# Kernel optimization log

Measured on AMD Instinct MI355X. Metric: run time of the kernel, lower is better.

## Reference

```python
import jax, jax.numpy as jnp
import numpy as np

HID = 128
FEAT = 16            # glob_in//(2+n_history) = (node_in-1)//4 = (edge_in-1)//4
N_GRAPHS = 512
N_NODES = 100000
N_EDGES = 400000
N_PER = 100000       # effects per branch (glob/node/edge)
A_TOTAL = 300000     # G.num_effects.sum()
EFF_PER_ACT = 4
NUM_ACTIONS = A_TOTAL // EFF_PER_ACT  # 75000 segments (static for jit)


def _lin(k, fan_in, fan_out):
    kw, kb = jax.random.split(k)
    s = 1.0 / np.sqrt(fan_in)
    W = jax.random.uniform(kw, (fan_in, fan_out), jnp.float32, -s, s)
    b = jax.random.uniform(kb, (fan_out,), jnp.float32, -s, s)
    return W, b


def setup_inputs() -> dict:
    key = jax.random.key(0)
    ks = jax.random.split(key, 16)
    globs = jax.random.normal(ks[0], (N_GRAPHS, HID), jnp.float32)
    nodes = jax.random.normal(ks[1], (N_NODES, HID), jnp.float32)
    edges = jax.random.normal(ks[2], (N_EDGES, HID), jnp.float32)
    action_globs = jax.random.normal(ks[3], (N_PER, FEAT), jnp.float32)
    action_nodes = jax.random.normal(ks[4], (N_PER, FEAT), jnp.float32)
    action_edges = jax.random.normal(ks[5], (N_PER, FEAT), jnp.float32)
    row = jax.random.randint(ks[6], (N_EDGES,), 0, N_NODES, jnp.int32)
    col = jax.random.randint(ks[7], (N_EDGES,), 0, N_NODES, jnp.int32)
    U = jax.random.randint(ks[8], (N_PER,), 0, N_GRAPHS, jnp.int32)
    V = jax.random.randint(ks[9], (N_PER,), 0, N_NODES, jnp.int32)
    E = jax.random.randint(ks[10], (N_PER,), 0, N_EDGES, jnp.int32)
    # disjoint write slots in the preallocated actions tensor
    UA = jnp.arange(N_PER, dtype=jnp.int32)
    VA = N_PER + jnp.arange(N_PER, dtype=jnp.int32)
    EA = 2 * N_PER + jnp.arange(N_PER, dtype=jnp.int32)
    # sorted per-effect action ids (4 effects per action)
    actions_batch = (jnp.arange(A_TOTAL, dtype=jnp.int32) // EFF_PER_ACT).astype(jnp.int32)
    glob_W, glob_b = _lin(ks[11], HID + FEAT, HID)
    node_W, node_b = _lin(ks[12], HID + FEAT, HID)
    e1_W, e1_b = _lin(ks[13], 2 * HID + FEAT, HID)
    e2_W, e2_b = _lin(ks[14], 2 * HID, HID)
    pol_W, pol_b = _lin(ks[15], HID, 1)
    return {
        "globs": globs, "nodes": nodes, "edges": edges,
        "action_globs": action_globs, "action_nodes": action_nodes, "action_edges": action_edges,
        "glob_W": glob_W, "glob_b": glob_b, "node_W": node_W, "node_b": node_b,
        "e1_W": e1_W, "e1_b": e1_b, "e2_W": e2_W, "e2_b": e2_b,
        "pol_W": pol_W, "pol_b": pol_b,
        "row": row, "col": col, "U": U, "UA": UA, "V": V, "VA": VA,
        "E": E, "EA": EA, "actions_batch": actions_batch,
    }


def _norm(batch):
    # torch norm(): consecutive group ids starting at batch[0]
    changed = (batch[1:] != batch[:-1]).astype(batch.dtype)
    return batch[0] + jnp.concatenate([jnp.zeros((1,), batch.dtype), jnp.cumsum(changed)])


def reference(globs, nodes, edges, action_globs, action_nodes, action_edges,
              glob_W, glob_b, node_W, node_b, e1_W, e1_b, e2_W, e2_b,
              pol_W, pol_b, row, col, U, UA, V, VA, E, EA, actions_batch):
    actions = jnp.zeros((A_TOTAL, HID), globs.dtype)
    # glob branch: gather globs -> small Linear -> index_put
    ga = jnp.concatenate([globs[U], action_globs], axis=1) @ glob_W + glob_b
    actions = actions.at[UA].set(ga)
    # node branch
    na = jnp.concatenate([nodes[V], action_nodes], axis=1) @ node_W + node_b
    actions = actions.at[VA].set(na)
    # edge branch: two chained Linears over gathered endpoint node feats
    EE = jnp.concatenate([nodes[row[E]], action_edges, nodes[col[E]]], axis=1) @ e1_W + e1_b
    ea = jnp.concatenate([edges[E], EE], axis=1) @ e2_W + e2_b
    actions = actions.at[EA].set(ea)
    # scatter_add segment reduction over action ids
    seg = _norm(actions_batch)
    agg = jax.ops.segment_sum(actions, seg, num_segments=NUM_ACTIONS)  # [NUM_ACTIONS, HID]
    return agg @ pol_W + pol_b  # [NUM_ACTIONS, 1]
```

## Files before the change

kernel.cpp:

```cpp
#include <hip/hip_runtime.h>

#define HID 128
#define FEAT 16
#define N_PER 100000
#define NUM_ACTIONS 75000
#define N_NODES 100000
#define N_GRAPHS 512

#define NSCAL_OFF 1024
#define GSCAL_OFF (NSCAL_OFF + 4 * N_NODES)
#define ESCAL_OFF (GSCAL_OFF + N_GRAPHS)
#define PSUM_OFF  (ESCAL_OFF + N_PER)

#define NB 760
#define EB 968
#define FB 288
#define GB 16
#define WORK_BLOCKS (NB + EB + FB + GB)

__device__ __forceinline__ float dot4(float4 a, float4 b) {
    return a.x * b.x + a.y * b.y + a.z * b.z + a.w * b.w;
}

template <int CTRL>
__device__ __forceinline__ float dpp_mov(float x) {
    return __int_as_float(__builtin_amdgcn_update_dpp(
        0, __float_as_int(x), CTRL, 0xF, 0xF, true));
}
__device__ __forceinline__ float red16(float x) {
    x += dpp_mov<0x111>(x);
    x += dpp_mov<0x112>(x);
    x += dpp_mov<0x114>(x);
    x += dpp_mov<0x118>(x);
    return x;
}
__device__ __forceinline__ float red32(float x) {
    x = red16(x);
    x += dpp_mov<0x142>(x);
    return x;
}
__device__ __forceinline__ float red64(float x) {
    x = red32(x);
    x += dpp_mov<0x143>(x);
    return x;
}

__global__ __launch_bounds__(1024) void fold_kernel(
    const float* __restrict__ glob_W, const float* __restrict__ glob_b,
    const float* __restrict__ node_W, const float* __restrict__ node_b,
    const float* __restrict__ e1_W,  const float* __restrict__ e1_b,
    const float* __restrict__ e2_W,  const float* __restrict__ e2_b,
    const float* __restrict__ pol_W, const float* __restrict__ pol_b,
    float* __restrict__ ws)
{
    __shared__ float qEE[HID];
    const int t = threadIdx.x, wave = t >> 6, lane = t & 63;
    const int bid = blockIdx.x;

    const bool needq = (bid >= 26 && bid <= 43);
    if (needq) {
        const int hw = t >> 5, s = t & 31;
        const float4 p4 = *(const float4*)&pol_W[4 * s];
        #pragma unroll
        for (int r = 0; r < 4; ++r) {
            const int k = hw + 32 * r;
            const float4 x = *(const float4*)&e2_W[(HID + k) * HID + 4 * s];
            float acc = red32(dot4(x, p4));
            if (s == 31) qEE[k] = acc;
        }
        __syncthreads();
    }

    const float2 p2 = *(const float2*)&pol_W[2 * lane];
    const int d = bid * 16 + wave;
    if (d == 691) {
        if (lane == 0) ws[691] = pol_b[0];
    } else if (d < 692) {
        float acc;
        if (d < 144) {
            const float2 x = *(const float2*)&glob_W[d * HID + 2 * lane];
            acc = x.x * p2.x + x.y * p2.y;
        } else if (d < 288) {
            const float2 x = *(const float2*)&node_W[(d - 144) * HID + 2 * lane];
            acc = x.x * p2.x + x.y * p2.y;
        } else if (d < 416) {
            const float2 x = *(const float2*)&e2_W[(d - 288) * HID + 2 * lane];
            acc = x.x * p2.x + x.y * p2.y;
        } else if (d < 688) {
            const float2 q2 = *(const float2*)&qEE[2 * lane];
            const float2 x  = *(const float2*)&e1_W[(d - 416) * HID + 2 * lane];
            acc = x.x * q2.x + x.y * q2.y;
        } else if (d == 688) {
            const float2 x = *(const float2*)&glob_b[2 * lane];
            acc = x.x * p2.x + x.y * p2.y;
        } else if (d == 689) {
            const float2 x = *(const float2*)&node_b[2 * lane];
            acc = x.x * p2.x + x.y * p2.y;
        } else {
            const float2 q2 = *(const float2*)&qEE[2 * lane];
            const float2 x1 = *(const float2*)&e1_b[2 * lane];
            const float2 x2 = *(const float2*)&e2_b[2 * lane];
            acc = x1.x * q2.x + x1.y * q2.y + x2.x * p2.x + x2.y * p2.y;
        }
        acc = red64(acc);
        if (lane == 63) ws[d] = acc;
    }
}

__global__ __launch_bounds__(256) void work_kernel(
    const float* __restrict__ nodes, const float* __restrict__ globs,
    const float* __restrict__ edges,
    const float* __restrict__ ag, const float* __restrict__ an,
    const float* __restrict__ ae,
    const int* __restrict__ E, float* __restrict__ ws)
{
    const int t = threadIdx.x, hw = t >> 5, s = t & 31;
    const int bid = blockIdx.x;

    if (bid < NB) {
        const float4 fr = *(const float4*)&ws[416 + 4 * s];
        const float4 fc = *(const float4*)&ws[560 + 4 * s];
        const float4 fn = *(const float4*)&ws[144 + 4 * s];
        for (int h = bid * 8 + hw; h < N_NODES; h += NB * 8) {
            const float4 x = *(const float4*)&nodes[h * HID + 4 * s];
            const float ar = red32(dot4(x, fr));
            const float ac = red32(dot4(x, fc));
            const float az = red32(dot4(x, fn));
            if (s == 31)
                *(float4*)&ws[NSCAL_OFF + 4 * h] = make_float4(ar, ac, az, 0.f);
        }
    } else if (bid < NB + EB) {
        const int eb = bid - NB;
        const float4 q4 = *(const float4*)&ws[288 + 4 * s];
        int g = eb * 8 + hw;
        const int stride = EB * 8;
        int e = (g < N_PER) ? E[g] : 0;
        while (g < N_PER) {
            const int gn = g + stride;
            const int en = (gn < N_PER) ? E[gn] : 0;
            const float4 x = *(const float4*)&edges[e * HID + 4 * s];
            const float acc = red32(dot4(x, q4));
            if (s == 31) ws[ESCAL_OFF + g] = acc;
            g = gn; e = en;
        }
    } else if (bid < NB + EB + FB) {
        const int fb = bid - NB - EB;
        const int qg = t >> 4, ql = t & 15;
        for (int a = fb * 16 + qg; a < NUM_ACTIONS; a += FB * 16) {
            const int br = a / 25000;
            const int gl = 4 * (a - br * 25000);
            const float* f = (br == 0) ? ag : (br == 1) ? an : ae;
            const int fbase = (br == 0) ? 128 : (br == 1) ? 272 : 544;
            const float4 fv = *(const float4*)&f[gl * FEAT + 4 * ql];
            const float4 wf = *(const float4*)&ws[fbase + 4 * (ql & 3)];
            const float p = red16(dot4(fv, wf));
            if (ql == 15) ws[PSUM_OFF + a] = p;
        }
    } else {
        const int gb = bid - NB - EB - FB;
        const float4 g4 = *(const float4*)&ws[4 * s];
        for (int u = gb * 8 + hw; u < N_GRAPHS; u += GB * 8) {
            const float4 x = *(const float4*)&globs[u * HID + 4 * s];
            const float a = red32(dot4(x, g4));
            if (s == 31) ws[GSCAL_OFF + u] = a;
        }
    }
}

__global__ __launch_bounds__(256) void final_kernel(
    const int* __restrict__ row, const int* __restrict__ col,
    const int* __restrict__ U, const int* __restrict__ V,
    const int* __restrict__ E,
    const float* __restrict__ ws, float* __restrict__ out)
{
    const int r = blockIdx.x * 256 + threadIdx.x;
    if (r >= 3 * N_PER) return;
    const int br = r / N_PER;
    const int g  = r - br * N_PER;

    float look, cb;
    if (br == 0) {
        look = ws[GSCAL_OFF + U[g]];
        cb = ws[688];
    } else if (br == 1) {
        look = ws[NSCAL_OFF + 4 * V[g] + 2];
        cb = ws[689];
    } else {
        const int e = E[g];
        look = ws[ESCAL_OFF + g]
             + ws[NSCAL_OFF + 4 * row[e] + 0]
             + ws[NSCAL_OFF + 4 * col[e] + 1];
        cb = ws[690];
    }
    float s4 = look;
    s4 += dpp_mov<0x111>(s4);
    s4 += dpp_mov<0x112>(s4);
    if ((threadIdx.x & 3) == 3) {
        const int a = r >> 2;
        out[a] = s4 + ws[PSUM_OFF + a] + 4.f * cb + ws[691];
    }
}

extern "C" void kernel_launch(void* const* d_in, const int* in_sizes, int n_in,
                              void* d_out, int out_size, void* d_ws, size_t ws_size,
                              hipStream_t stream)
{
    const float* globs  = (const float*)d_in[0];
    const float* nodes  = (const float*)d_in[1];
    const float* edges  = (const float*)d_in[2];
    const float* ag     = (const float*)d_in[3];
    const float* an     = (const float*)d_in[4];
    const float* ae     = (const float*)d_in[5];
    const float* glob_W = (const float*)d_in[6];
    const float* glob_b = (const float*)d_in[7];
    const float* node_W = (const float*)d_in[8];
    const float* node_b = (const float*)d_in[9];
    const float* e1_W   = (const float*)d_in[10];
    const float* e1_b   = (const float*)d_in[11];
    const float* e2_W   = (const float*)d_in[12];
    const float* e2_b   = (const float*)d_in[13];
    const float* pol_W  = (const float*)d_in[14];
    const float* pol_b  = (const float*)d_in[15];
    const int*   row    = (const int*)d_in[16];
    const int*   col    = (const int*)d_in[17];
    const int*   U      = (const int*)d_in[18];
    const int*   V      = (const int*)d_in[20];
    const int*   E      = (const int*)d_in[22];

    float* ws  = (float*)d_ws;
    float* out = (float*)d_out;

    hipLaunchKernelGGL(fold_kernel, dim3(44), dim3(1024), 0, stream,
                       glob_W, glob_b, node_W, node_b, e1_W, e1_b, e2_W, e2_b,
                       pol_W, pol_b, ws);
    hipLaunchKernelGGL(work_kernel, dim3(WORK_BLOCKS), dim3(256), 0, stream,
                       nodes, globs, edges, ag, an, ae, E, ws);
    hipLaunchKernelGGL(final_kernel, dim3((3 * N_PER + 255) / 256), dim3(256),
                       0, stream, row, col, U, V, E, ws, out);
}
```

Baseline: 35.68 us.

## Unroll node/edge row loops by two and compute one action per thread in final kernel

```diff
diff --git a/kernel.cpp b/kernel.cpp
--- a/kernel.cpp
+++ b/kernel.cpp
@@ -12,9 +12,9 @@
 #define ESCAL_OFF (GSCAL_OFF + N_GRAPHS)
 #define PSUM_OFF  (ESCAL_OFF + N_PER)
 
-#define NB 760
-#define EB 968
-#define FB 288
+#define NB 720
+#define EB 1040
+#define FB 256
 #define GB 16
 #define WORK_BLOCKS (NB + EB + FB + GB)
 
@@ -121,27 +121,45 @@
         const float4 fr = *(const float4*)&ws[416 + 4 * s];
         const float4 fc = *(const float4*)&ws[560 + 4 * s];
         const float4 fn = *(const float4*)&ws[144 + 4 * s];
-        for (int h = bid * 8 + hw; h < N_NODES; h += NB * 8) {
-            const float4 x = *(const float4*)&nodes[h * HID + 4 * s];
-            const float ar = red32(dot4(x, fr));
-            const float ac = red32(dot4(x, fc));
-            const float az = red32(dot4(x, fn));
-            if (s == 31)
-                *(float4*)&ws[NSCAL_OFF + 4 * h] = make_float4(ar, ac, az, 0.f);
+        const int stride = NB * 8;
+        for (int h0 = bid * 8 + hw; h0 < N_NODES; h0 += 2 * stride) {
+            const int h1 = h0 + stride;
+            const float4 x0 = *(const float4*)&nodes[h0 * HID + 4 * s];
+            float4 x1 = make_float4(0.f, 0.f, 0.f, 0.f);
+            if (h1 < N_NODES) x1 = *(const float4*)&nodes[h1 * HID + 4 * s];
+            const float ar0 = red32(dot4(x0, fr));
+            const float ac0 = red32(dot4(x0, fc));
+            const float az0 = red32(dot4(x0, fn));
+            const float ar1 = red32(dot4(x1, fr));
+            const float ac1 = red32(dot4(x1, fc));
+            const float az1 = red32(dot4(x1, fn));
+            if (s == 31) {
+                *(float4*)&ws[NSCAL_OFF + 4 * h0] = make_float4(ar0, ac0, az0, 0.f);
+                if (h1 < N_NODES)
+                    *(float4*)&ws[NSCAL_OFF + 4 * h1] = make_float4(ar1, ac1, az1, 0.f);
+            }
         }
     } else if (bid < NB + EB) {
         const int eb = bid - NB;
         const float4 q4 = *(const float4*)&ws[288 + 4 * s];
+        const int stride = EB * 8;
         int g = eb * 8 + hw;
-        const int stride = EB * 8;
-        int e = (g < N_PER) ? E[g] : 0;
+        int e0 = (g < N_PER) ? E[g] : 0;
+        int e1 = (g + stride < N_PER) ? E[g + stride] : 0;
         while (g < N_PER) {
-            const int gn = g + stride;
-            const int en = (gn < N_PER) ? E[gn] : 0;
-            const float4 x = *(const float4*)&edges[e * HID + 4 * s];
-            const float acc = red32(dot4(x, q4));
-            if (s == 31) ws[ESCAL_OFF + g] = acc;
-            g = gn; e = en;
+            const int gn = g + 2 * stride;
+            const int en0 = (gn < N_PER) ? E[gn] : 0;
+            const int en1 = (gn + stride < N_PER) ? E[gn + stride] : 0;
+            const float4 x0 = *(const float4*)&edges[e0 * HID + 4 * s];
+            float4 x1 = make_float4(0.f, 0.f, 0.f, 0.f);
+            if (g + stride < N_PER) x1 = *(const float4*)&edges[e1 * HID + 4 * s];
+            const float a0 = red32(dot4(x0, q4));
+            const float a1 = red32(dot4(x1, q4));
+            if (s == 31) {
+                ws[ESCAL_OFF + g] = a0;
+                if (g + stride < N_PER) ws[ESCAL_OFF + g + stride] = a1;
+            }
+            g = gn; e0 = en0; e1 = en1;
         }
     } else if (bid < NB + EB + FB) {
         const int fb = bid - NB - EB;
@@ -173,32 +191,31 @@
     const int* __restrict__ E,
     const float* __restrict__ ws, float* __restrict__ out)
 {
-    const int r = blockIdx.x * 256 + threadIdx.x;
-    if (r >= 3 * N_PER) return;
-    const int br = r / N_PER;
-    const int g  = r - br * N_PER;
-
-    float look, cb;
-    if (br == 0) {
-        look = ws[GSCAL_OFF + U[g]];
-        cb = ws[688];
-    } else if (br == 1) {
-        look = ws[NSCAL_OFF + 4 * V[g] + 2];
-        cb = ws[689];
+    const int a = blockIdx.x * 256 + threadIdx.x;
+    if (a >= NUM_ACTIONS) return;
+
+    float sum;
+    if (a < 25000) {
+        const int4 u4 = *(const int4*)&U[4 * a];
+        sum = ws[GSCAL_OFF + u4.x] + ws[GSCAL_OFF + u4.y]
+            + ws[GSCAL_OFF + u4.z] + ws[GSCAL_OFF + u4.w]
+            + 4.f * ws[688];
+    } else if (a < 50000) {
+        const int4 v4 = *(const int4*)&V[4 * (a - 25000)];
+        sum = ws[NSCAL_OFF + 4 * v4.x + 2] + ws[NSCAL_OFF + 4 * v4.y + 2]
+            + ws[NSCAL_OFF + 4 * v4.z + 2] + ws[NSCAL_OFF + 4 * v4.w + 2]
+            + 4.f * ws[689];
     } else {
-        const int e = E[g];
-        look = ws[ESCAL_OFF + g]
-             + ws[NSCAL_OFF + 4 * row[e] + 0]
-             + ws[NSCAL_OFF + 4 * col[e] + 1];
-        cb = ws[690];
-    }
-    float s4 = look;
-    s4 += dpp_mov<0x111>(s4);
-    s4 += dpp_mov<0x112>(s4);
-    if ((threadIdx.x & 3) == 3) {
-        const int a = r >> 2;
-        out[a] = s4 + ws[PSUM_OFF + a] + 4.f * cb + ws[691];
-    }
+        const int g = 4 * (a - 50000);
+        const int4 e4 = *(const int4*)&E[g];
+        const float4 es = *(const float4*)&ws[ESCAL_OFF + g];
+        sum = es.x + es.y + es.z + es.w + 4.f * ws[690];
+        sum += ws[NSCAL_OFF + 4 * row[e4.x] + 0] + ws[NSCAL_OFF + 4 * col[e4.x] + 1];
+        sum += ws[NSCAL_OFF + 4 * row[e4.y] + 0] + ws[NSCAL_OFF + 4 * col[e4.y] + 1];
+        sum += ws[NSCAL_OFF + 4 * row[e4.z] + 0] + ws[NSCAL_OFF + 4 * col[e4.z] + 1];
+        sum += ws[NSCAL_OFF + 4 * row[e4.w] + 0] + ws[NSCAL_OFF + 4 * col[e4.w] + 1];
+    }
+    out[a] = sum + ws[PSUM_OFF + a] + ws[691];
 }
 
 extern "C" void kernel_launch(void* const* d_in, const int* in_sizes, int n_in,
@@ -235,6 +252,6 @@
                        pol_W, pol_b, ws);
     hipLaunchKernelGGL(work_kernel, dim3(WORK_BLOCKS), dim3(256), 0, stream,
                        nodes, globs, edges, ag, an, ae, E, ws);
-    hipLaunchKernelGGL(final_kernel, dim3((3 * N_PER + 255) / 256), dim3(256),
+    hipLaunchKernelGGL(final_kernel, dim3((NUM_ACTIONS + 255) / 256), dim3(256),
                        0, stream, row, col, U, V, E, ws, out);
 }
```

Result: slower. 38.46 us (+7.8%).
